# Kernel tuning notes

Hardware: AMD Instinct MI355X
Metric: run time of the kernel (lower is better)

Reference implementation:

```python
import jax, jax.numpy as jnp
import numpy as np
import math

C, H, L, V = 1024, 16, 2, 32000
D = C // H  # head_dim = 64
FF = 4 * C
B, T = 1, 2048
EPS = 1e-5

def _alibi_slopes(n_heads):
    start = 2 ** (-2 ** (-(math.log2(n_heads) - 3)))
    return np.array([start * start ** i for i in range(n_heads)], dtype=np.float32)

SLOPES = jnp.asarray(_alibi_slopes(H))

def _sym_ln(x, w, b):
    # per-head-channel LayerNorm over head_dim, scalar scale/bias per head
    xh = x.reshape(x.shape[0], x.shape[1], H, D)
    mu = xh.mean(-1, keepdims=True)
    var = ((xh - mu) ** 2).mean(-1, keepdims=True)
    n = (xh - mu) / jnp.sqrt(var + EPS)
    n = n * w[None, None, :, None] + b[None, None, :, None]
    return n.reshape(x.shape)

def _alibi_bias(t):
    pos = jnp.arange(t)[None, :] - jnp.arange(t)[:, None]  # j - i
    pos = jnp.minimum(pos, 0).astype(jnp.float32)
    return SLOPES[:, None, None] * pos[None, :, :]  # (H, T, T)

def _block(x, ln1_w, ln1_b, ln2_w, ln2_b, attn_w, attn_b, v_tmp, proj_tmp, fc_w, fc_b, pw, pb):
    b_, t_, _ = x.shape
    h_in = _sym_ln(x, ln1_w, ln1_b)
    qk = h_in @ attn_w.T + attn_b  # (B, T, 2C)
    q, k = jnp.split(qk, 2, axis=-1)
    # Kronecker/block-diagonal V: per-head (head_dim x head_dim) matmul, x @ M^T per head
    xh = h_in.reshape(b_, t_, H, D)
    v = jnp.einsum('bthd,hed->bthe', xh, v_tmp)  # (B, T, H, D)
    q = q.reshape(b_, t_, H, D).transpose(0, 2, 1, 3)
    k = k.reshape(b_, t_, H, D).transpose(0, 2, 1, 3)
    v = v.transpose(0, 2, 1, 3)
    scale = 1.0 / math.sqrt(D)
    scores = jnp.einsum('bhqd,bhkd->bhqk', q, k) * scale
    scores = scores + _alibi_bias(t_)[None]  # note: no causal mask in original code
    att = jax.nn.softmax(scores, axis=-1)
    y = jnp.einsum('bhqk,bhkd->bhqd', att, v)
    y = y.transpose(0, 2, 1, 3)  # (B, T, H, D)
    y = jnp.einsum('bthd,hed->bthe', y, proj_tmp).reshape(b_, t_, C)
    x = x + y
    h2 = _sym_ln(x, ln2_w, ln2_b)
    f = jax.nn.gelu(h2 @ fc_w.T + fc_b, approximate=False)
    x = x + (f @ pw.T + pb)
    return x

def setup_inputs() -> dict:
    key = jax.random.key(0)
    ks = jax.random.split(key, 12)
    s = 0.02
    return {
        'idx': jax.random.randint(ks[0], (B, T), 0, V, dtype=jnp.int32),
        'wte': jax.random.normal(ks[1], (V, C), jnp.float32) * s,
        'ln1_w': jnp.ones((L, H), jnp.float32),
        'ln1_b': jnp.zeros((L, H), jnp.float32),
        'ln2_w': jnp.ones((L, H), jnp.float32),
        'ln2_b': jnp.zeros((L, H), jnp.float32),
        'lnf_w': jnp.ones((H,), jnp.float32),
        'lnf_b': jnp.zeros((H,), jnp.float32),
        'attn_w': jax.random.normal(ks[2], (L, 2 * C, C), jnp.float32) * s,
        'attn_b': jnp.zeros((L, 2 * C), jnp.float32),
        'v_tmp': jax.random.normal(ks[3], (L, H, D, D), jnp.float32) * s,
        'proj_tmp': jax.random.normal(ks[4], (L, H, D, D), jnp.float32) * s,
        'fc_w': jax.random.normal(ks[5], (L, FF, C), jnp.float32) * s,
        'fc_b': jnp.zeros((L, FF), jnp.float32),
        'proj_w': jax.random.normal(ks[6], (L, C, FF), jnp.float32) * s,
        'proj_b': jnp.zeros((L, C), jnp.float32),
    }

def reference(idx, wte, ln1_w, ln1_b, ln2_w, ln2_b, lnf_w, lnf_b,
              attn_w, attn_b, v_tmp, proj_tmp, fc_w, fc_b, proj_w, proj_b):
    x = wte[idx]  # (B, T, C)
    for l in range(L):
        x = _block(x, ln1_w[l], ln1_b[l], ln2_w[l], ln2_b[l],
                   attn_w[l], attn_b[l], v_tmp[l], proj_tmp[l],
                   fc_w[l], fc_b[l], proj_w[l], proj_b[l])
    x = _sym_ln(x, lnf_w, lnf_b)
    logits = x @ wte.T  # tied lm_head
    return logits
```

## Files before the change

### kernel.cpp

```cpp
#include <hip/hip_runtime.h>
#include <cstdint>
#include <cstddef>

#define T_SEQ 2048
#define C_DIM 1024
#define H_HEADS 16
#define D_HEAD 64
#define FF_DIM 4096
#define V_VOCAB 32000
#define L_LAYERS 2

typedef unsigned short u16;
typedef short bf16x8 __attribute__((ext_vector_type(8)));
typedef float f32x4 __attribute__((ext_vector_type(4)));

__device__ inline u16 f2bf(float f) {
  unsigned u = __float_as_uint(f);
  u += 0x7fffu + ((u >> 16) & 1u);
  return (u16)(u >> 16);
}
__device__ inline float bf2f(u16 h) { return __uint_as_float(((unsigned)h) << 16); }

#define OFF_WTEBF   0ULL
#define OFF_ATTNBF  65536000ULL
#define OFF_FCBF    73924608ULL
#define OFF_PRJBF   90701824ULL
#define OFF_X       107479040ULL
#define OFF_HBF     115867648ULL
#define OFF_QKBF    120061952ULL
#define OFF_VT      128450560ULL
#define OFF_FBF     141033472ULL
#define OFF_VWBF    157810688ULL
#define OFF_PWBF    158072832ULL
#define ARENA_BYTES 158334976ULL

__device__ __align__(1024) unsigned char g_arena[ARENA_BYTES];

__global__ void cvt_all_k(const float4* __restrict__ sw, const float4* __restrict__ s0,
                          const float4* __restrict__ s1, const float4* __restrict__ s2,
                          const float4* __restrict__ s3, const float4* __restrict__ s4,
                          ushort4* __restrict__ dw, ushort4* __restrict__ d0,
                          ushort4* __restrict__ d1, ushort4* __restrict__ d2,
                          ushort4* __restrict__ d3, ushort4* __restrict__ d4) {
  int g = blockIdx.x * 256 + threadIdx.x;
  const float4* s; ushort4* d; int off;
  if (g < 8192000)       { s = sw; d = dw; off = g; }
  else {
    int g2 = g - 8192000;
    if (g2 < 1048576)      { s = s0; d = d0; off = g2; }
    else if (g2 < 3145728) { s = s1; d = d1; off = g2 - 1048576; }
    else if (g2 < 5242880) { s = s2; d = d2; off = g2 - 3145728; }
    else if (g2 < 5275648) { s = s3; d = d3; off = g2 - 5242880; }
    else                   { s = s4; d = d4; off = g2 - 5275648; }
  }
  float4 v = s[off];
  d[off] = make_ushort4(f2bf(v.x), f2bf(v.y), f2bf(v.z), f2bf(v.w));
}

__global__ void embed_k(const int* __restrict__ idx, const float4* __restrict__ wte,
                        float4* __restrict__ x) {
  int t = blockIdx.x;
  int r = idx[t];
  x[(size_t)t * 256 + threadIdx.x] = wte[(size_t)r * 256 + threadIdx.x];
}

__global__ void symln_k(const float* __restrict__ x, const float* __restrict__ w,
                        const float* __restrict__ b, u16* __restrict__ out) {
  int t = blockIdx.x;
  int wv = threadIdx.x >> 6, lane = threadIdx.x & 63;
  #pragma unroll
  for (int hh = 0; hh < 4; hh++) {
    int h = wv * 4 + hh;
    float v = x[(size_t)t * C_DIM + h * 64 + lane];
    float s = v, s2 = v * v;
    #pragma unroll
    for (int m = 32; m; m >>= 1) { s += __shfl_xor(s, m); s2 += __shfl_xor(s2, m); }
    float mu = s * (1.f / 64.f);
    float var = s2 * (1.f / 64.f) - mu * mu;
    float n = (v - mu) * rsqrtf(var + 1e-5f) * w[h] + b[h];
    out[(size_t)t * C_DIM + h * 64 + lane] = f2bf(n);
  }
}

template <int NROWS, int ROWBYTES, int WAVES>
__device__ inline void stage_rows(u16* lds, const u16* __restrict__ g, int ld,
                                  int wid, int lane) {
  constexpr int PASSES = (NROWS * ROWBYTES) / (WAVES * 1024);
  #pragma unroll
  for (int i = 0; i < PASSES; i++) {
    int base = (i * WAVES + wid) * 1024;
    int o = base + lane * 16;
    int u = o ^ (((o / ROWBYTES) & 7) << 4);
    int row = u / ROWBYTES, colb = u % ROWBYTES;
    const u16* src = g + (size_t)row * ld + (colb >> 1);
    __builtin_amdgcn_global_load_lds((const __attribute__((address_space(1))) void*)src,
                                     (__attribute__((address_space(3))) void*)(lds + base / 2),
                                     16, 0, 0);
  }
}

__device__ inline void stage_pass(u16* lds, const u16* __restrict__ g, int ld,
                                  int i, int wid, int lane) {
  int base = (i * 8 + wid) * 1024;
  int o = base + lane * 16;
  int u = o ^ (((o >> 7) & 7) << 4);
  int row = u >> 7, colb = u & 127;
  const u16* src = g + (size_t)row * ld + (colb >> 1);
  __builtin_amdgcn_global_load_lds((const __attribute__((address_space(1))) void*)src,
                                   (__attribute__((address_space(3))) void*)(lds + base / 2),
                                   16, 0, 0);
}

__global__ __launch_bounds__(256) void flash_k(const u16* __restrict__ qk,
                                               const u16* __restrict__ vt,
                                               const u16* __restrict__ pw,
                                               float* __restrict__ x) {
  int h = blockIdx.y;
  int q0 = blockIdx.x * 64;
  int tid = threadIdx.x, wid = tid >> 6, lane = tid & 63;
  int g4 = lane >> 4, l15 = lane & 15;
  __shared__ u16 Kl[128 * 64];
  __shared__ u16 Vl[64 * 128];
  __shared__ u16 Pl[64 * 128];
  float slope = exp2f(-0.5f * (float)(h + 1));

  bf16x8 qf[2];
  const u16* qb = qk + (size_t)(q0 + wid * 16) * 2048 + h * 64;
  #pragma unroll
  for (int kk = 0; kk < 2; kk++)
    qf[kk] = *(const bf16x8*)(qb + (size_t)l15 * 2048 + kk * 32 + g4 * 8);

  float lsum = 0.f;
  f32x4 oacc[4];
  #pragma unroll
  for (int n = 0; n < 4; n++) oacc[n] = (f32x4){0.f, 0.f, 0.f, 0.f};

  const u16* kbase = qk + 1024 + h * 64;
  const u16* vbase = vt + (size_t)h * 64 * T_SEQ;
  int myq = q0 + wid * 16 + l15;

  for (int kt = 0; kt < T_SEQ / 128; kt++) {
    int k0 = kt * 128;
    stage_rows<128, 128, 4>(Kl, kbase + (size_t)k0 * 2048, 2048, wid, lane);
    stage_rows<64, 256, 4>(Vl, vbase + k0, T_SEQ, wid, lane);
    __syncthreads();

    f32x4 s[8];
    #pragma unroll
    for (int n = 0; n < 8; n++) s[n] = (f32x4){0.f, 0.f, 0.f, 0.f};
    #pragma unroll
    for (int kk = 0; kk < 2; kk++) {
      #pragma unroll
      for (int n = 0; n < 8; n++) {
        int r = n * 16 + l15;
        int b = (r * 128 + kk * 64 + g4 * 16) ^ ((r & 7) << 4);
        bf16x8 kf = *(const bf16x8*)((const char*)Kl + b);
        s[n] = __builtin_amdgcn_mfma_f32_16x16x32_bf16(kf, qf[kk], s[n], 0, 0, 0);
      }
    }

    float fd = (float)(k0 + g4 * 4 - myq);
    int pr = wid * 16 + l15;
    #pragma unroll
    for (int n = 0; n < 8; n++) {
      float p[4];
      #pragma unroll
      for (int i = 0; i < 4; i++) {
        float dj = fd + (float)(n * 16 + i);
        float a2 = fmaf(slope, fminf(dj, 0.f), -8.f);
        p[i] = __expf(fmaf(s[n][i], 0.125f, a2));
        lsum += p[i];
      }
      unsigned lo, hi;
      asm("v_cvt_pk_bf16_f32 %0, %1, %2" : "=v"(lo) : "v"(p[0]), "v"(p[1]));
      asm("v_cvt_pk_bf16_f32 %0, %1, %2" : "=v"(hi) : "v"(p[2]), "v"(p[3]));
      int b = (pr * 256 + n * 32 + g4 * 8) ^ ((pr & 7) << 4);
      *(uint2*)((char*)Pl + b) = make_uint2(lo, hi);
    }

    #pragma unroll
    for (int kk = 0; kk < 4; kk++) {
      int pb = (pr * 256 + kk * 64 + g4 * 16) ^ ((pr & 7) << 4);
      bf16x8 pa = *(const bf16x8*)((const char*)Pl + pb);
      #pragma unroll
      for (int n = 0; n < 4; n++) {
        int d = n * 16 + l15;
        int vb = (d * 256 + kk * 64 + g4 * 16) ^ ((d & 7) << 4);
        bf16x8 vf = *(const bf16x8*)((const char*)Vl + vb);
        oacc[n] = __builtin_amdgcn_mfma_f32_16x16x32_bf16(pa, vf, oacc[n], 0, 0, 0);
      }
    }
    __syncthreads();
  }

  lsum += __shfl_xor(lsum, 16);
  lsum += __shfl_xor(lsum, 32);
  float linv[4];
  #pragma unroll
  for (int i = 0; i < 4; i++) linv[i] = 1.f / __shfl(lsum, g4 * 4 + i);

  stage_rows<64, 128, 4>(Kl, pw + (size_t)h * 4096, 64, wid, lane);
  #pragma unroll
  for (int n = 0; n < 4; n++)
    #pragma unroll
    for (int i = 0; i < 4; i++) {
      int pr = wid * 16 + g4 * 4 + i;
      int b = (pr * 256 + (n * 16 + l15) * 2) ^ ((pr & 7) << 4);
      *(u16*)((char*)Pl + b) = f2bf(oacc[n][i] * linv[i]);
    }
  __syncthreads();

  f32x4 acc2[4];
  #pragma unroll
  for (int n = 0; n < 4; n++) acc2[n] = (f32x4){0.f, 0.f, 0.f, 0.f};
  #pragma unroll
  for (int kk = 0; kk < 2; kk++) {
    int pr = wid * 16 + l15;
    int ab = (pr * 256 + kk * 64 + g4 * 16) ^ ((pr & 7) << 4);
    bf16x8 af = *(const bf16x8*)((const char*)Pl + ab);
    #pragma unroll
    for (int n = 0; n < 4; n++) {
      int r = n * 16 + l15;
      int wb = (r * 128 + kk * 64 + g4 * 16) ^ ((r & 7) << 4);
      bf16x8 wf = *(const bf16x8*)((const char*)Kl + wb);
      acc2[n] = __builtin_amdgcn_mfma_f32_16x16x32_bf16(af, wf, acc2[n], 0, 0, 0);
    }
  }
  float* xb = x + (size_t)(q0 + wid * 16) * C_DIM + h * 64;
  #pragma unroll
  for (int n = 0; n < 4; n++)
    #pragma unroll
    for (int i = 0; i < 4; i++)
      xb[(size_t)(g4 * 4 + i) * C_DIM + n * 16 + l15] += acc2[n][i];
}

#define ASM_VMCNT0 asm volatile("s_waitcnt vmcnt(0)" ::: "memory")

__global__ __launch_bounds__(512, 1) void gemm256_k(const u16* __restrict__ A, int lda,
                                                    const u16* __restrict__ B, int ldb,
                                                    float* __restrict__ C, int ldc,
                                                    int K, int MT) {
  extern __shared__ u16 sm[];
  u16* lsA = sm;
  u16* lsB = sm + 32768;
  int tid = threadIdx.x, wid = tid >> 6, lane = tid & 63;
  int g4 = lane >> 4, l15 = lane & 15;
  int wm = wid >> 2, wn = wid & 3;
  int nwg = gridDim.x, lin = blockIdx.x;
  int chunk = nwg >> 3;
  int w = (lin & 7) * chunk + (lin >> 3);
  int by = w % MT, bx = w / MT;
  const u16* Ab = A + (size_t)(by * 256) * lda;
  const u16* Bb = B + (size_t)(bx * 256) * ldb;

  f32x4 acc[8][4];
  #pragma unroll
  for (int m = 0; m < 8; m++)
    #pragma unroll
    for (int n = 0; n < 4; n++) acc[m][n] = (f32x4){0.f, 0.f, 0.f, 0.f};

  int NT = K >> 6;
  stage_rows<256, 128, 8>(lsA, Ab, lda, wid, lane);
  stage_rows<256, 128, 8>(lsB, Bb, ldb, wid, lane);

  for (int t = 0; t < NT; ++t) {
    int cur = t & 1;
    const char* cA = (const char*)(lsA + cur * 16384);
    const char* cB = (const char*)(lsB + cur * 16384);
    u16* nAl = lsA + (cur ^ 1) * 16384;
    u16* nBl = lsB + (cur ^ 1) * 16384;
    const u16* gA = Ab + (t + 1) * 64;
    const u16* gB = Bb + (t + 1) * 64;
    bool pf = (t + 1 < NT);

    ASM_VMCNT0;
    __builtin_amdgcn_s_barrier();
    __builtin_amdgcn_sched_barrier(0);

    bf16x8 bfr[4], af[4];
    #pragma unroll
    for (int ph = 0; ph < 4; ++ph) {
      const int kk = ph >> 1, mh = ph & 1;
      if (mh == 0) {
        #pragma unroll
        for (int n = 0; n < 4; n++) {
          int r = wn * 64 + n * 16 + l15;
          bfr[n] = *(const bf16x8*)(cB + ((r * 128 + kk * 64 + g4 * 16) ^ ((r & 7) << 4)));
        }
      }
      #pragma unroll
      for (int m = 0; m < 4; m++) {
        int r = wm * 128 + mh * 64 + m * 16 + l15;
        af[m] = *(const bf16x8*)(cA + ((r * 128 + kk * 64 + g4 * 16) ^ ((r & 7) << 4)));
      }
      if (pf) {
        if (ph == 0) { stage_pass(nAl, gA, lda, 0, wid, lane);
                       stage_pass(nAl, gA, lda, 1, wid, lane);
                       stage_pass(nBl, gB, ldb, 0, wid, lane); }
        else if (ph == 1) { stage_pass(nAl, gA, lda, 2, wid, lane);
                            stage_pass(nAl, gA, lda, 3, wid, lane);
                            stage_pass(nBl, gB, ldb, 1, wid, lane); }
        else if (ph == 2) { stage_pass(nBl, gB, ldb, 2, wid, lane);
                            stage_pass(nBl, gB, ldb, 3, wid, lane); }
      }
      __builtin_amdgcn_s_setprio(1);
      #pragma unroll
      for (int m = 0; m < 4; m++)
        #pragma unroll
        for (int n = 0; n < 4; n++)
          acc[mh * 4 + m][n] =
              __builtin_amdgcn_mfma_f32_16x16x32_bf16(af[m], bfr[n], acc[mh * 4 + m][n], 0, 0, 0);
      __builtin_amdgcn_s_setprio(0);
      __builtin_amdgcn_s_barrier();
    }
  }

  int gr0 = by * 256 + wm * 128, gc0 = bx * 256 + wn * 64;
  #pragma unroll
  for (int m = 0; m < 8; m++)
    #pragma unroll
    for (int n = 0; n < 4; n++)
      #pragma unroll
      for (int i = 0; i < 4; i++)
        C[(size_t)(gr0 + m * 16 + g4 * 4 + i) * ldc + gc0 + n * 16 + l15] = acc[m][n][i];
}

template <int BM, int BN, int WM, int WN, int EPI, int MT, int GRID>
__global__ void gemm_nt(const u16* __restrict__ A, int lda, long long sA,
                        const u16* __restrict__ B, int ldb, long long sB,
                        void* __restrict__ C, int ldc, long long sC,
                        int K, const float* __restrict__ bias,
                        const float* __restrict__ resid, int ldr) {
  constexpr int RM = BM / WM, RN = BN / WN;
  constexpr int MR = RM / 16, NR = RN / 16;
  __shared__ u16 lsA[BM * 64];
  __shared__ u16 lsB[BN * 64];
  int tid = threadIdx.x, wid = tid >> 6, lane = tid & 63;
  int wm = wid / WN, wn = wid % WN;
  int lin, z;
  if constexpr (GRID == 1) {
    lin = blockIdx.x; z = blockIdx.y;
  } else {
    int nwg = gridDim.x, l0 = blockIdx.x;
    int chunk = nwg >> 3;
    lin = (l0 & 7) * chunk + (l0 >> 3);
    z = 0;
  }
  int by = lin % MT, bx = lin / MT;
  int row0 = by * BM, col0 = bx * BN;
  const u16* Ab = A + (size_t)z * sA + (size_t)row0 * lda;
  const u16* Bb = B + (size_t)z * sB + (size_t)col0 * ldb;
  size_t cz = (size_t)z * sC;

  f32x4 acc[MR][NR];
  #pragma unroll
  for (int m = 0; m < MR; m++)
    #pragma unroll
    for (int n = 0; n < NR; n++) acc[m][n] = (f32x4){0.f, 0.f, 0.f, 0.f};

  for (int k0 = 0; k0 < K; k0 += 64) {
    stage_rows<BM, 128, 4>(lsA, Ab + k0, lda, wid, lane);
    stage_rows<BN, 128, 4>(lsB, Bb + k0, ldb, wid, lane);
    __syncthreads();
    #pragma unroll
    for (int kk = 0; kk < 2; kk++) {
      bf16x8 af[MR], bfr[NR];
      #pragma unroll
      for (int m = 0; m < MR; m++) {
        int r = wm * RM + m * 16 + (lane & 15);
        int bofs = (r * 128 + kk * 64 + ((lane >> 4) * 16)) ^ ((r & 7) << 4);
        af[m] = *(const bf16x8*)((const char*)lsA + bofs);
      }
      #pragma unroll
      for (int n = 0; n < NR; n++) {
        int r = wn * RN + n * 16 + (lane & 15);
        int bofs = (r * 128 + kk * 64 + ((lane >> 4) * 16)) ^ ((r & 7) << 4);
        bfr[n] = *(const bf16x8*)((const char*)lsB + bofs);
      }
      #pragma unroll
      for (int m = 0; m < MR; m++)
        #pragma unroll
        for (int n = 0; n < NR; n++)
          acc[m][n] = __builtin_amdgcn_mfma_f32_16x16x32_bf16(af[m], bfr[n], acc[m][n], 0, 0, 0);
    }
    __syncthreads();
  }

  int rbase = row0 + wm * RM, cbase = col0 + wn * RN;
  #pragma unroll
  for (int m = 0; m < MR; m++)
    #pragma unroll
    for (int n = 0; n < NR; n++)
      #pragma unroll
      for (int i = 0; i < 4; i++) {
        int gr = rbase + m * 16 + ((lane >> 4) * 4) + i;
        int gc = cbase + n * 16 + (lane & 15);
        size_t idx = cz + (size_t)gr * ldc + gc;
        float v = acc[m][n][i];
        if constexpr (EPI == 0) {
          ((float*)C)[idx] = v;
        } else if constexpr (EPI == 1) {
          v += bias[gc];
          ((u16*)C)[idx] = f2bf(v);
        } else if constexpr (EPI == 2) {
          ((u16*)C)[idx] = f2bf(v);
        } else if constexpr (EPI == 3) {
          v += bias[gc];
          v = 0.5f * v * (1.f + erff(v * 0.70710678118654752f));
          ((u16*)C)[idx] = f2bf(v);
        } else if constexpr (EPI == 4) {
          v += bias[gc] + resid[(size_t)gr * ldr + gc];
          ((float*)C)[idx] = v;
        } else {
          ((float*)C)[idx] += v;
        }
      }
}

extern "C" void kernel_launch(void* const* d_in, const int* in_sizes, int n_in,
                              void* d_out, int out_size, void* d_ws, size_t ws_size,
                              hipStream_t stream) {
  (void)in_sizes; (void)n_in; (void)out_size; (void)d_ws; (void)ws_size;
  const int*   idx    = (const int*)d_in[0];
  const float* wte    = (const float*)d_in[1];
  const float* ln1w   = (const float*)d_in[2];
  const float* ln1b   = (const float*)d_in[3];
  const float* ln2w   = (const float*)d_in[4];
  const float* ln2b   = (const float*)d_in[5];
  const float* lnfw   = (const float*)d_in[6];
  const float* lnfb   = (const float*)d_in[7];
  const float* attw   = (const float*)d_in[8];
  const float* attb   = (const float*)d_in[9];
  const float* vtmp   = (const float*)d_in[10];
  const float* ptmp   = (const float*)d_in[11];
  const float* fcw    = (const float*)d_in[12];
  const float* fcb    = (const float*)d_in[13];
  const float* prjw   = (const float*)d_in[14];
  const float* prjb   = (const float*)d_in[15];
  float* out = (float*)d_out;

  unsigned char* ar = nullptr;
  hipGetSymbolAddress((void**)&ar, HIP_SYMBOL(g_arena));
  u16*   wtebf  = (u16*)(ar + OFF_WTEBF);
  u16*   attnbf = (u16*)(ar + OFF_ATTNBF);
  u16*   fcbf   = (u16*)(ar + OFF_FCBF);
  u16*   prjbf  = (u16*)(ar + OFF_PRJBF);
  float* x      = (float*)(ar + OFF_X);
  u16*   hbf    = (u16*)(ar + OFF_HBF);
  u16*   qkbf   = (u16*)(ar + OFF_QKBF);
  u16*   vt     = (u16*)(ar + OFF_VT);
  u16*   fbf    = (u16*)(ar + OFF_FBF);
  u16*   vwbf   = (u16*)(ar + OFF_VWBF);
  u16*   pwbf   = (u16*)(ar + OFF_PWBF);

  hipFuncSetAttribute((const void*)gemm256_k,
                      hipFuncAttributeMaxDynamicSharedMemorySize, 131072);

  cvt_all_k<<<dim3(52736), 256, 0, stream>>>(
      (const float4*)wte, (const float4*)attw, (const float4*)fcw,
      (const float4*)prjw, (const float4*)vtmp, (const float4*)ptmp,
      (ushort4*)wtebf, (ushort4*)attnbf, (ushort4*)fcbf,
      (ushort4*)prjbf, (ushort4*)vwbf, (ushort4*)pwbf);

  embed_k<<<dim3(T_SEQ), 256, 0, stream>>>(idx, (const float4*)wte, (float4*)x);

  for (int l = 0; l < L_LAYERS; l++) {
    symln_k<<<dim3(T_SEQ), 256, 0, stream>>>(x, ln1w + l * H_HEADS, ln1b + l * H_HEADS, hbf);
    gemm_nt<64, 128, 2, 2, 1, 32, 0><<<dim3((2 * C_DIM / 128) * (T_SEQ / 64)), 256, 0, stream>>>(
        hbf, C_DIM, 0, attnbf + (size_t)l * 2 * C_DIM * C_DIM, C_DIM, 0,
        qkbf, 2 * C_DIM, 0, C_DIM, attb + l * 2 * C_DIM, nullptr, 0);
    gemm_nt<64, 128, 2, 2, 2, 1, 1><<<dim3(T_SEQ / 128, H_HEADS), 256, 0, stream>>>(
        vwbf + (size_t)l * H_HEADS * 4096, 64, 4096, hbf, C_DIM, 64,
        vt, T_SEQ, (long long)64 * T_SEQ, 64, nullptr, nullptr, 0);
    flash_k<<<dim3(T_SEQ / 64, H_HEADS), 256, 0, stream>>>(
        qkbf, vt, pwbf + (size_t)l * H_HEADS * 4096, x);
    symln_k<<<dim3(T_SEQ), 256, 0, stream>>>(x, ln2w + l * H_HEADS, ln2b + l * H_HEADS, hbf);
    gemm_nt<64, 128, 2, 2, 3, 32, 0><<<dim3((FF_DIM / 128) * (T_SEQ / 64)), 256, 0, stream>>>(
        hbf, C_DIM, 0, fcbf + (size_t)l * FF_DIM * C_DIM, C_DIM, 0,
        fbf, FF_DIM, 0, C_DIM, fcb + l * FF_DIM, nullptr, 0);
    gemm_nt<64, 128, 2, 2, 4, 32, 0><<<dim3((C_DIM / 128) * (T_SEQ / 64)), 256, 0, stream>>>(
        fbf, FF_DIM, 0, prjbf + (size_t)l * C_DIM * FF_DIM, FF_DIM, 0,
        x, C_DIM, 0, FF_DIM, prjb + l * C_DIM, x, C_DIM);
  }
  symln_k<<<dim3(T_SEQ), 256, 0, stream>>>(x, lnfw, lnfb, hbf);
  gemm256_k<<<dim3((V_VOCAB / 256) * (T_SEQ / 256)), 512, 131072, stream>>>(
      hbf, C_DIM, wtebf, C_DIM, out, V_VOCAB, C_DIM, T_SEQ / 256);
}
```

Before: 539.6 us.

## Fuse per-head LayerNorm into embedding, attention and MLP-projection epilogues

Removes the standalone symln kernels by computing the per-head LayerNorm inside the epilogues that produce x: the embedding gather, the flash attention residual update, and a new EPI mode of the down-projection GEMM that also prepares the next layer's or the final LN input. Each wave already holds a full 64-column head slice, so the statistics come from 16-lane shuffles. This saves kernel launches and a re-read of x, at the cost of extra register pressure and work in those epilogues.

```diff
diff --git a/kernel.cpp b/kernel.cpp
--- a/kernel.cpp
+++ b/kernel.cpp
@@ -57,29 +57,23 @@
   d[off] = make_ushort4(f2bf(v.x), f2bf(v.y), f2bf(v.z), f2bf(v.w));
 }
 
-__global__ void embed_k(const int* __restrict__ idx, const float4* __restrict__ wte,
-                        float4* __restrict__ x) {
-  int t = blockIdx.x;
+__global__ void embed_ln_k(const int* __restrict__ idx, const float4* __restrict__ wte,
+                           float4* __restrict__ x, const float* __restrict__ w,
+                           const float* __restrict__ b, ushort4* __restrict__ out) {
+  int t = blockIdx.x, tid = threadIdx.x;
   int r = idx[t];
-  x[(size_t)t * 256 + threadIdx.x] = wte[(size_t)r * 256 + threadIdx.x];
-}
-
-__global__ void symln_k(const float* __restrict__ x, const float* __restrict__ w,
-                        const float* __restrict__ b, u16* __restrict__ out) {
-  int t = blockIdx.x;
-  int wv = threadIdx.x >> 6, lane = threadIdx.x & 63;
-  #pragma unroll
-  for (int hh = 0; hh < 4; hh++) {
-    int h = wv * 4 + hh;
-    float v = x[(size_t)t * C_DIM + h * 64 + lane];
-    float s = v, s2 = v * v;
-    #pragma unroll
-    for (int m = 32; m; m >>= 1) { s += __shfl_xor(s, m); s2 += __shfl_xor(s2, m); }
-    float mu = s * (1.f / 64.f);
-    float var = s2 * (1.f / 64.f) - mu * mu;
-    float n = (v - mu) * rsqrtf(var + 1e-5f) * w[h] + b[h];
-    out[(size_t)t * C_DIM + h * 64 + lane] = f2bf(n);
-  }
+  float4 v = wte[(size_t)r * 256 + tid];
+  x[(size_t)t * 256 + tid] = v;
+  float s = v.x + v.y + v.z + v.w;
+  float s2 = v.x * v.x + v.y * v.y + v.z * v.z + v.w * v.w;
+  #pragma unroll
+  for (int m = 1; m <= 8; m <<= 1) { s += __shfl_xor(s, m); s2 += __shfl_xor(s2, m); }
+  int h = tid >> 4;
+  float mu = s * (1.f / 64.f), var = s2 * (1.f / 64.f) - mu * mu;
+  float rs = rsqrtf(var + 1e-5f) * w[h], lb = b[h];
+  out[(size_t)t * 256 + tid] =
+      make_ushort4(f2bf((v.x - mu) * rs + lb), f2bf((v.y - mu) * rs + lb),
+                   f2bf((v.z - mu) * rs + lb), f2bf((v.w - mu) * rs + lb));
 }
 
 template <int NROWS, int ROWBYTES, int WAVES>
@@ -114,7 +108,10 @@
 __global__ __launch_bounds__(256) void flash_k(const u16* __restrict__ qk,
                                                const u16* __restrict__ vt,
                                                const u16* __restrict__ pw,
-                                               float* __restrict__ x) {
+                                               float* __restrict__ x,
+                                               const float* __restrict__ ln2w,
+                                               const float* __restrict__ ln2b,
+                                               u16* __restrict__ hout) {
   int h = blockIdx.y;
   int q0 = blockIdx.x * 64;
   int tid = threadIdx.x, wid = tid >> 6, lane = tid & 63;
@@ -226,12 +223,33 @@
       acc2[n] = __builtin_amdgcn_mfma_f32_16x16x32_bf16(af, wf, acc2[n], 0, 0, 0);
     }
   }
+
   float* xb = x + (size_t)(q0 + wid * 16) * C_DIM + h * 64;
+  u16* hb = hout + (size_t)(q0 + wid * 16) * C_DIM + h * 64;
+  float xv[4][4];
   #pragma unroll
   for (int n = 0; n < 4; n++)
     #pragma unroll
-    for (int i = 0; i < 4; i++)
-      xb[(size_t)(g4 * 4 + i) * C_DIM + n * 16 + l15] += acc2[n][i];
+    for (int i = 0; i < 4; i++) {
+      size_t o = (size_t)(g4 * 4 + i) * C_DIM + n * 16 + l15;
+      float t = xb[o] + acc2[n][i];
+      xb[o] = t;
+      xv[n][i] = t;
+    }
+  float lw = ln2w[h], lb = ln2b[h];
+  #pragma unroll
+  for (int i = 0; i < 4; i++) {
+    float s = 0.f, s2 = 0.f;
+    #pragma unroll
+    for (int n = 0; n < 4; n++) { float t = xv[n][i]; s += t; s2 += t * t; }
+    #pragma unroll
+    for (int m = 1; m <= 8; m <<= 1) { s += __shfl_xor(s, m); s2 += __shfl_xor(s2, m); }
+    float mu = s * (1.f / 64.f), var = s2 * (1.f / 64.f) - mu * mu;
+    float rs = rsqrtf(var + 1e-5f) * lw;
+    #pragma unroll
+    for (int n = 0; n < 4; n++)
+      hb[(size_t)(g4 * 4 + i) * C_DIM + n * 16 + l15] = f2bf((xv[n][i] - mu) * rs + lb);
+  }
 }
 
 #define ASM_VMCNT0 asm volatile("s_waitcnt vmcnt(0)" ::: "memory")
@@ -330,7 +348,9 @@
                         const u16* __restrict__ B, int ldb, long long sB,
                         void* __restrict__ C, int ldc, long long sC,
                         int K, const float* __restrict__ bias,
-                        const float* __restrict__ resid, int ldr) {
+                        const float* __restrict__ resid, int ldr,
+                        const float* __restrict__ lnw, const float* __restrict__ lnb,
+                        u16* __restrict__ hout) {
   constexpr int RM = BM / WM, RN = BN / WN;
   constexpr int MR = RM / 16, NR = RN / 16;
   __shared__ u16 lsA[BM * 64];
@@ -387,34 +407,63 @@
   }
 
   int rbase = row0 + wm * RM, cbase = col0 + wn * RN;
-  #pragma unroll
-  for (int m = 0; m < MR; m++)
-    #pragma unroll
-    for (int n = 0; n < NR; n++)
+  if constexpr (EPI == 6) {
+    float vv[MR][NR][4];
+    #pragma unroll
+    for (int m = 0; m < MR; m++)
+      #pragma unroll
+      for (int n = 0; n < NR; n++)
+        #pragma unroll
+        for (int i = 0; i < 4; i++) {
+          int gr = rbase + m * 16 + ((lane >> 4) * 4) + i;
+          int gc = cbase + n * 16 + (lane & 15);
+          float v = acc[m][n][i] + bias[gc] + resid[(size_t)gr * ldr + gc];
+          vv[m][n][i] = v;
+          ((float*)C)[(size_t)gr * ldc + gc] = v;
+        }
+    int h = cbase >> 6;
+    float lw = lnw[h], lb = lnb[h];
+    #pragma unroll
+    for (int m = 0; m < MR; m++)
       #pragma unroll
       for (int i = 0; i < 4; i++) {
+        float s = 0.f, s2 = 0.f;
+        #pragma unroll
+        for (int n = 0; n < NR; n++) { float t = vv[m][n][i]; s += t; s2 += t * t; }
+        #pragma unroll
+        for (int msk = 1; msk <= 8; msk <<= 1) { s += __shfl_xor(s, msk); s2 += __shfl_xor(s2, msk); }
+        float mu = s * (1.f / 64.f), var = s2 * (1.f / 64.f) - mu * mu;
+        float rs = rsqrtf(var + 1e-5f) * lw;
         int gr = rbase + m * 16 + ((lane >> 4) * 4) + i;
-        int gc = cbase + n * 16 + (lane & 15);
-        size_t idx = cz + (size_t)gr * ldc + gc;
-        float v = acc[m][n][i];
-        if constexpr (EPI == 0) {
-          ((float*)C)[idx] = v;
-        } else if constexpr (EPI == 1) {
-          v += bias[gc];
-          ((u16*)C)[idx] = f2bf(v);
-        } else if constexpr (EPI == 2) {
-          ((u16*)C)[idx] = f2bf(v);
-        } else if constexpr (EPI == 3) {
-          v += bias[gc];
-          v = 0.5f * v * (1.f + erff(v * 0.70710678118654752f));
-          ((u16*)C)[idx] = f2bf(v);
-        } else if constexpr (EPI == 4) {
-          v += bias[gc] + resid[(size_t)gr * ldr + gc];
-          ((float*)C)[idx] = v;
-        } else {
-          ((float*)C)[idx] += v;
+        #pragma unroll
+        for (int n = 0; n < NR; n++) {
+          int gc = cbase + n * 16 + (lane & 15);
+          hout[(size_t)gr * C_DIM + gc] = f2bf((vv[m][n][i] - mu) * rs + lb);
         }
       }
+  } else {
+    #pragma unroll
+    for (int m = 0; m < MR; m++)
+      #pragma unroll
+      for (int n = 0; n < NR; n++)
+        #pragma unroll
+        for (int i = 0; i < 4; i++) {
+          int gr = rbase + m * 16 + ((lane >> 4) * 4) + i;
+          int gc = cbase + n * 16 + (lane & 15);
+          size_t idx = cz + (size_t)gr * ldc + gc;
+          float v = acc[m][n][i];
+          if constexpr (EPI == 1) {
+            v += bias[gc];
+            ((u16*)C)[idx] = f2bf(v);
+          } else if constexpr (EPI == 2) {
+            ((u16*)C)[idx] = f2bf(v);
+          } else if constexpr (EPI == 3) {
+            v += bias[gc];
+            v = 0.5f * v * (1.f + erff(v * 0.70710678118654752f));
+            ((u16*)C)[idx] = f2bf(v);
+          }
+        }
+  }
 }
 
 extern "C" void kernel_launch(void* const* d_in, const int* in_sizes, int n_in,
@@ -462,27 +511,32 @@
       (ushort4*)wtebf, (ushort4*)attnbf, (ushort4*)fcbf,
       (ushort4*)prjbf, (ushort4*)vwbf, (ushort4*)pwbf);
 
-  embed_k<<<dim3(T_SEQ), 256, 0, stream>>>(idx, (const float4*)wte, (float4*)x);
+  embed_ln_k<<<dim3(T_SEQ), 256, 0, stream>>>(idx, (const float4*)wte, (float4*)x,
+                                              ln1w, ln1b, (ushort4*)hbf);
 
   for (int l = 0; l < L_LAYERS; l++) {
-    symln_k<<<dim3(T_SEQ), 256, 0, stream>>>(x, ln1w + l * H_HEADS, ln1b + l * H_HEADS, hbf);
     gemm_nt<64, 128, 2, 2, 1, 32, 0><<<dim3((2 * C_DIM / 128) * (T_SEQ / 64)), 256, 0, stream>>>(
         hbf, C_DIM, 0, attnbf + (size_t)l * 2 * C_DIM * C_DIM, C_DIM, 0,
-        qkbf, 2 * C_DIM, 0, C_DIM, attb + l * 2 * C_DIM, nullptr, 0);
+        qkbf, 2 * C_DIM, 0, C_DIM, attb + l * 2 * C_DIM, nullptr, 0,
+        nullptr, nullptr, nullptr);
     gemm_nt<64, 128, 2, 2, 2, 1, 1><<<dim3(T_SEQ / 128, H_HEADS), 256, 0, stream>>>(
         vwbf + (size_t)l * H_HEADS * 4096, 64, 4096, hbf, C_DIM, 64,
-        vt, T_SEQ, (long long)64 * T_SEQ, 64, nullptr, nullptr, 0);
+        vt, T_SEQ, (long long)64 * T_SEQ, 64, nullptr, nullptr, 0,
+        nullptr, nullptr, nullptr);
     flash_k<<<dim3(T_SEQ / 64, H_HEADS), 256, 0, stream>>>(
-        qkbf, vt, pwbf + (size_t)l * H_HEADS * 4096, x);
-    symln_k<<<dim3(T_SEQ), 256, 0, stream>>>(x, ln2w + l * H_HEADS, ln2b + l * H_HEADS, hbf);
+        qkbf, vt, pwbf + (size_t)l * H_HEADS * 4096, x,
+        ln2w + l * H_HEADS, ln2b + l * H_HEADS, hbf);
     gemm_nt<64, 128, 2, 2, 3, 32, 0><<<dim3((FF_DIM / 128) * (T_SEQ / 64)), 256, 0, stream>>>(
         hbf, C_DIM, 0, fcbf + (size_t)l * FF_DIM * C_DIM, C_DIM, 0,
-        fbf, FF_DIM, 0, C_DIM, fcb + l * FF_DIM, nullptr, 0);
-    gemm_nt<64, 128, 2, 2, 4, 32, 0><<<dim3((C_DIM / 128) * (T_SEQ / 64)), 256, 0, stream>>>(
+        fbf, FF_DIM, 0, C_DIM, fcb + l * FF_DIM, nullptr, 0,
+        nullptr, nullptr, nullptr);
+    const float* nw = (l + 1 < L_LAYERS) ? ln1w + (l + 1) * H_HEADS : lnfw;
+    const float* nb = (l + 1 < L_LAYERS) ? ln1b + (l + 1) * H_HEADS : lnfb;
+    gemm_nt<64, 128, 2, 2, 6, 32, 0><<<dim3((C_DIM / 128) * (T_SEQ / 64)), 256, 0, stream>>>(
         fbf, FF_DIM, 0, prjbf + (size_t)l * C_DIM * FF_DIM, FF_DIM, 0,
-        x, C_DIM, 0, FF_DIM, prjb + l * C_DIM, x, C_DIM);
-  }
-  symln_k<<<dim3(T_SEQ), 256, 0, stream>>>(x, lnfw, lnfb, hbf);
+        x, C_DIM, 0, FF_DIM, prjb + l * C_DIM, x, C_DIM,
+        nw, nb, hbf);
+  }
   gemm256_k<<<dim3((V_VOCAB / 256) * (T_SEQ / 256)), 512, 131072, stream>>>(
       hbf, C_DIM, wtebf, C_DIM, out, V_VOCAB, C_DIM, T_SEQ / 256);
 }
```

Measured after the change: 516.8 us. -4.2%, faster.
